# Optimization experiments

Measured on AMD Instinct MI355X. Metric: run time of the kernel, lower is better.

Reference implementation:

```python
import jax, jax.numpy as jnp
import numpy as np

HID = 768
HEADS = 12
HEAD_LEN = HID // HEADS
SCALE_INV = 1.0 / np.sqrt(HEAD_LEN).astype(np.float32)


def setup_inputs() -> dict:
    key = jax.random.key(0)
    ks = jax.random.split(key, 5)
    std = 1.0 / np.sqrt(HID)
    return {
        "x": jax.random.normal(ks[0], (1, 4096, HID), dtype=jnp.float32),
        "w_q": jax.random.normal(ks[1], (HID, HID), dtype=jnp.float32) * std,
        "w_k": jax.random.normal(ks[2], (HID, HID), dtype=jnp.float32) * std,
        "w_v": jax.random.normal(ks[3], (HID, HID), dtype=jnp.float32) * std,
        "w_fc": jax.random.normal(ks[4], (HID, HID), dtype=jnp.float32) * std,
    }


def reference(x, w_q, w_k, w_v, w_fc):
    B, S, D = x.shape
    # torch Linear weight layout [out, in]: y = x @ W.T
    def proj_heads(w):
        y = jnp.einsum("bsd,ed->bse", x, w)
        return y.reshape(B, S, HEADS, HEAD_LEN).transpose(0, 2, 1, 3)  # bhsd
    q = proj_heads(w_q)
    k = proj_heads(w_k)
    v = proj_heads(w_v)
    scores = SCALE_INV * jnp.einsum("bhqd,bhkd->bhqk", q, k)
    attn = jax.nn.softmax(scores, axis=-1)
    out = jnp.einsum("bhqk,bhkd->bhqd", attn, v)
    out = out.transpose(0, 2, 1, 3).reshape(B, S, D)
    return jnp.einsum("bsd,ed->bse", out, w_fc)
```

## Files before the change

### kernel.cpp

```cpp
#include <hip/hip_runtime.h>
#include <hip/hip_bf16.h>

#define S_LEN 4096
#define HID 768
#define NHEAD 12
#define HL 64
#define PSS 72

typedef __attribute__((ext_vector_type(8))) short short8;
typedef __attribute__((ext_vector_type(4))) float f32x4;
using bf16 = __hip_bfloat16;

__device__ __forceinline__ void gl2lds16(const void* g, void* l) {
  __builtin_amdgcn_global_load_lds((__attribute__((address_space(1))) void*)(g),
                                   (__attribute__((address_space(3))) void*)(l),
                                   16, 0, 0);
}

__device__ __forceinline__ f32x4 mfma_bf16(short8 a, short8 b, f32x4 c) {
  return __builtin_amdgcn_mfma_f32_16x16x32_bf16(a, b, c, 0, 0, 0);
}

__device__ __forceinline__ void storeC(float* C, long idx, float v) { C[idx] = v; }
__device__ __forceinline__ void storeC(bf16* C, long idx, float v) { C[idx] = __float2bfloat16(v); }

#define BAR() asm volatile("s_waitcnt lgkmcnt(0)\n\ts_barrier" ::: "memory")

__global__ __launch_bounds__(256) void cvt_all(
    const float* __restrict__ x, const float* __restrict__ wq,
    const float* __restrict__ wk, const float* __restrict__ wv,
    const float* __restrict__ wfc, bf16* __restrict__ xb, bf16* __restrict__ wqb,
    bf16* __restrict__ wkb, bf16* __restrict__ wvb, bf16* __restrict__ wfcb) {
  const long NX = (long)S_LEN * HID;
  const long NW = (long)HID * HID;
  long i = ((long)blockIdx.x * 256 + threadIdx.x) * 4;
  const float* src;
  bf16* dst;
  long off;
  if (i < NX) {
    src = x; dst = xb; off = i;
  } else {
    long j = i - NX;
    int wsel = (int)(j / NW);
    off = j - (long)wsel * NW;
    src = wsel == 0 ? wq : wsel == 1 ? wk : wsel == 2 ? wv : wfc;
    dst = wsel == 0 ? wqb : wsel == 1 ? wkb : wsel == 2 ? wvb : wfcb;
  }
  float4 v = *(const float4*)(src + off);
  bf16 h0 = __float2bfloat16(v.x), h1 = __float2bfloat16(v.y);
  bf16 h2 = __float2bfloat16(v.z), h3 = __float2bfloat16(v.w);
  ushort4 o;
  o.x = *(unsigned short*)&h0; o.y = *(unsigned short*)&h1;
  o.z = *(unsigned short*)&h2; o.w = *(unsigned short*)&h3;
  *(ushort4*)(dst + off) = o;
}

template <typename OT>
__global__ __launch_bounds__(256) void gemm_bt(
    const bf16* __restrict__ A, const bf16* __restrict__ B0,
    const bf16* __restrict__ B1, const bf16* __restrict__ B2,
    OT* __restrict__ C0, OT* __restrict__ C1, OT* __restrict__ C2, float qscale) {
  constexpr int K = HID;
  __shared__ __align__(16) bf16 As[128 * 32];
  __shared__ __align__(16) bf16 Bs[128 * 32];
  const int z = blockIdx.z;
  const bf16* B = (z == 0) ? B0 : (z == 1) ? B1 : B2;
  OT* C = (z == 0) ? C0 : (z == 1) ? C1 : C2;
  const float sc = (z == 0) ? qscale : 1.0f;
  const int bm = blockIdx.y, bn = blockIdx.x;
  const int t = threadIdx.x, lane = t & 63, w = t >> 6;
  const int wm = w >> 1, wn = w & 1;
  const int q4 = lane >> 4, c16 = lane & 15;
  const int srow = lane >> 2, scol = (lane & 3) * 8;
  const bf16* Ab = A + (long)bm * 128 * K;
  const bf16* Bb = B + (long)bn * 128 * K;
  f32x4 acc[4][4] = {};
  for (int k0 = 0; k0 < K; k0 += 32) {
#pragma unroll
    for (int r = 0; r < 2; ++r) {
      int rowb = r * 64 + w * 16;
      gl2lds16(Ab + (long)(rowb + srow) * K + k0 + scol, &As[rowb * 32]);
      gl2lds16(Bb + (long)(rowb + srow) * K + k0 + scol, &Bs[rowb * 32]);
    }
    __syncthreads();
    short8 af[4], bfv[4];
#pragma unroll
    for (int i = 0; i < 4; ++i)
      af[i] = *(const short8*)&As[(wm * 64 + i * 16 + c16) * 32 + q4 * 8];
#pragma unroll
    for (int j = 0; j < 4; ++j)
      bfv[j] = *(const short8*)&Bs[(wn * 64 + j * 16 + c16) * 32 + q4 * 8];
#pragma unroll
    for (int i = 0; i < 4; ++i)
#pragma unroll
      for (int j = 0; j < 4; ++j)
        acc[i][j] = mfma_bf16(af[i], bfv[j], acc[i][j]);
    __syncthreads();
  }
  const long crow0 = (long)bm * 128 + wm * 64;
  const int ccol0 = bn * 128 + wn * 64;
#pragma unroll
  for (int i = 0; i < 4; ++i)
#pragma unroll
    for (int j = 0; j < 4; ++j)
#pragma unroll
      for (int r = 0; r < 4; ++r) {
        long row = crow0 + i * 16 + q4 * 4 + r;
        int col = ccol0 + j * 16 + c16;
        storeC(C, row * HID + col, sc * acc[i][j][r]);
      }
}

__global__ __launch_bounds__(256) void gemm_fc(const bf16* __restrict__ A,
                                               const bf16* __restrict__ B,
                                               float* __restrict__ C) {
  __shared__ __align__(16) bf16 As[128 * 32];
  __shared__ __align__(16) bf16 Bs[64 * 32];
  const int bm = blockIdx.y, bn = blockIdx.x;
  const int t = threadIdx.x, lane = t & 63, w = t >> 6;
  const int q4 = lane >> 4, c16 = lane & 15;
  const int srow = lane >> 2, scol = (lane & 3) * 8;
  const bf16* Ab = A + (long)bm * 128 * HID;
  const bf16* Bb = B + (long)bn * 64 * HID;
  f32x4 acc[2][4] = {};
  for (int k0 = 0; k0 < HID; k0 += 32) {
#pragma unroll
    for (int r = 0; r < 2; ++r) {
      int rowb = w * 32 + r * 16;
      gl2lds16(Ab + (long)(rowb + srow) * HID + k0 + scol, &As[rowb * 32]);
    }
    gl2lds16(Bb + (long)(w * 16 + srow) * HID + k0 + scol, &Bs[w * 16 * 32]);
    __syncthreads();
    short8 af[2], bfv[4];
#pragma unroll
    for (int i = 0; i < 2; ++i)
      af[i] = *(const short8*)&As[(w * 32 + i * 16 + c16) * 32 + q4 * 8];
#pragma unroll
    for (int j = 0; j < 4; ++j)
      bfv[j] = *(const short8*)&Bs[(j * 16 + c16) * 32 + q4 * 8];
#pragma unroll
    for (int i = 0; i < 2; ++i)
#pragma unroll
      for (int j = 0; j < 4; ++j)
        acc[i][j] = mfma_bf16(af[i], bfv[j], acc[i][j]);
    __syncthreads();
  }
#pragma unroll
  for (int i = 0; i < 2; ++i)
#pragma unroll
    for (int j = 0; j < 4; ++j)
#pragma unroll
      for (int r = 0; r < 4; ++r) {
        long row = (long)bm * 128 + w * 32 + i * 16 + q4 * 4 + r;
        int col = bn * 64 + j * 16 + c16;
        C[row * HID + col] = acc[i][j][r];
      }
}

__global__ __launch_bounds__(256) void transpose_v(const bf16* __restrict__ V,
                                                   bf16* __restrict__ Vt) {
  __shared__ unsigned short tile[64][65];
  const int bs = blockIdx.x * 64;
  const int be = blockIdx.y * 64;
  const int t = threadIdx.x;
#pragma unroll
  for (int p = 0; p < 4; ++p) {
    int i = p * 256 + t;
    int r = i >> 4;
    int c = (i & 15) * 4;
    ushort4 v = *(const ushort4*)((const unsigned short*)V + (long)(bs + r) * HID + be + c);
    tile[r][c] = v.x; tile[r][c + 1] = v.y; tile[r][c + 2] = v.z; tile[r][c + 3] = v.w;
  }
  __syncthreads();
#pragma unroll
  for (int p = 0; p < 4; ++p) {
    int i = p * 256 + t;
    int r = i >> 4;
    int c = (i & 15) * 4;
    ushort4 v;
    v.x = tile[c][r]; v.y = tile[c + 1][r]; v.z = tile[c + 2][r]; v.w = tile[c + 3][r];
    *(ushort4*)((unsigned short*)Vt + (long)(be + r) * S_LEN + bs + c) = v;
  }
}

__global__ __launch_bounds__(256, 3) void flash_attn(const bf16* __restrict__ Q,
                                                     const bf16* __restrict__ Kg,
                                                     const bf16* __restrict__ Vt,
                                                     bf16* __restrict__ O) {
  __shared__ __align__(16) bf16 Ps[64 * PSS];
  __shared__ float Lred[4][64];
  const int qt = blockIdx.x, h = blockIdx.y;
  const int t = threadIdx.x, lane = t & 63, w = t >> 6;
  const int q4 = lane >> 4, c16 = lane & 15;
  const int s0 = qt * 64;

  short8 qf[2][4];
  {
    const bf16* Qb = Q + (long)(s0 + c16) * HID + h * HL + q4 * 8;
#pragma unroll
    for (int j = 0; j < 4; ++j)
#pragma unroll
      for (int ks = 0; ks < 2; ++ks)
        qf[ks][j] = *(const short8*)(Qb + (long)j * 16 * HID + ks * 32);
  }
  const bf16* kp = Kg + (long)(w * 16 + c16) * HID + h * HL + q4 * 8;
  const bf16* vp = Vt + (long)(h * HL + w * 16 + c16) * S_LEN + q4 * 8;

  float l_part[4] = {0.f, 0.f, 0.f, 0.f};
  f32x4 o_acc[4] = {};
  short8 kf0 = *(const short8*)(kp), kf1 = *(const short8*)(kp + 32);
  short8 vf0 = *(const short8*)(vp), vf1 = *(const short8*)(vp + 32);

  for (int kt = 0; kt < S_LEN / 64; ++kt) {
    f32x4 sacc[4] = {};
#pragma unroll
    for (int j = 0; j < 4; ++j) sacc[j] = mfma_bf16(kf0, qf[0][j], sacc[j]);
#pragma unroll
    for (int j = 0; j < 4; ++j) sacc[j] = mfma_bf16(kf1, qf[1][j], sacc[j]);

    const bf16* kpn = kp + 64 * HID;
    const bf16* vpn = vp + 64;
    if (kt == S_LEN / 64 - 1) { kpn = kp; vpn = vp; }
    short8 nk0 = *(const short8*)(kpn), nk1 = *(const short8*)(kpn + 32);
    short8 nv0 = *(const short8*)(vpn), nv1 = *(const short8*)(vpn + 32);

#pragma unroll
    for (int j = 0; j < 4; ++j) {
      float p0 = __builtin_amdgcn_exp2f(sacc[j][0]);
      float p1 = __builtin_amdgcn_exp2f(sacc[j][1]);
      float p2 = __builtin_amdgcn_exp2f(sacc[j][2]);
      float p3 = __builtin_amdgcn_exp2f(sacc[j][3]);
      l_part[j] += (p0 + p1) + (p2 + p3);
      bf16 b0 = __float2bfloat16(p0), b1 = __float2bfloat16(p1);
      bf16 b2 = __float2bfloat16(p2), b3 = __float2bfloat16(p3);
      short4 pk;
      pk.x = *(short*)&b0; pk.y = *(short*)&b1; pk.z = *(short*)&b2; pk.w = *(short*)&b3;
      *(short4*)&Ps[(j * 16 + c16) * PSS + w * 16 + q4 * 4] = pk;
    }
    BAR();

#pragma unroll
    for (int ks = 0; ks < 2; ++ks) {
      short8 vfk = ks ? vf1 : vf0;
#pragma unroll
      for (int j = 0; j < 4; ++j) {
        short8 pf = *(const short8*)&Ps[(j * 16 + c16) * PSS + ks * 32 + q4 * 8];
        o_acc[j] = mfma_bf16(vfk, pf, o_acc[j]);
      }
    }
    BAR();

    kf0 = nk0; kf1 = nk1; vf0 = nv0; vf1 = nv1;
    kp = kpn; vp = vpn;
  }

#pragma unroll
  for (int j = 0; j < 4; ++j) {
    float s = l_part[j];
    s += __shfl_xor(s, 16, 64);
    s += __shfl_xor(s, 32, 64);
    Lred[w][j * 16 + c16] = s;
  }
  BAR();
#pragma unroll
  for (int j = 0; j < 4; ++j) {
    int q = j * 16 + c16;
    float lt = Lred[0][q] + Lred[1][q] + Lred[2][q] + Lred[3][q];
    float rl = 1.0f / lt;
    float v0 = o_acc[j][0] * rl, v1 = o_acc[j][1] * rl;
    float v2 = o_acc[j][2] * rl, v3 = o_acc[j][3] * rl;
    bf16 b0 = __float2bfloat16(v0), b1 = __float2bfloat16(v1);
    bf16 b2 = __float2bfloat16(v2), b3 = __float2bfloat16(v3);
    short4 pk;
    pk.x = *(short*)&b0; pk.y = *(short*)&b1; pk.z = *(short*)&b2; pk.w = *(short*)&b3;
    *(short4*)&O[(long)(s0 + q) * HID + h * HL + w * 16 + q4 * 4] = pk;
  }
}

extern "C" void kernel_launch(void* const* d_in, const int* in_sizes, int n_in,
                              void* d_out, int out_size, void* d_ws, size_t ws_size,
                              hipStream_t stream) {
  const float* x = (const float*)d_in[0];
  const float* wq = (const float*)d_in[1];
  const float* wk = (const float*)d_in[2];
  const float* wv = (const float*)d_in[3];
  const float* wfc = (const float*)d_in[4];
  float* out = (float*)d_out;

  const long NBIG = (long)S_LEN * HID * sizeof(bf16);
  const long NWB = (long)HID * HID * sizeof(bf16);
  char* p = (char*)d_ws;
  bf16* xb = (bf16*)p;   p += NBIG;
  bf16* wqb = (bf16*)p;  p += NWB;
  bf16* wkb = (bf16*)p;  p += NWB;
  bf16* wvb = (bf16*)p;  p += NWB;
  bf16* wfcb = (bf16*)p; p += NWB;
  bf16* Qb = (bf16*)p;   p += NBIG;
  bf16* Kb = (bf16*)p;   p += NBIG;
  bf16* Vb = (bf16*)p;   p += NBIG;
  bf16* Vtb = (bf16*)p;  p += NBIG;
  bf16* Ob = (bf16*)p;   p += NBIG;

  const float c1 = 0.125f * 1.44269504088896340736f;

  const long total4 = ((long)S_LEN * HID + 4L * HID * HID) / 4;
  cvt_all<<<(int)(total4 / 256), 256, 0, stream>>>(x, wq, wk, wv, wfc, xb, wqb, wkb,
                                                   wvb, wfcb);
  gemm_bt<bf16><<<dim3(HID / 128, S_LEN / 128, 3), 256, 0, stream>>>(
      xb, wqb, wkb, wvb, Qb, Kb, Vb, c1);
  transpose_v<<<dim3(S_LEN / 64, HID / 64), 256, 0, stream>>>(Vb, Vtb);
  flash_attn<<<dim3(S_LEN / 64, NHEAD), 256, 0, stream>>>(Qb, Kb, Vtb, Ob);
  gemm_fc<<<dim3(HID / 64, S_LEN / 128), 256, 0, stream>>>(Ob, wfcb, out);
}
```

Measured before the change: 211.3 us.

## Keep P in registers for PV MFMA and remap blocks by XCD

New measurement: 277.3 us. 31.2% more time.

```diff
diff --git a/kernel.cpp b/kernel.cpp
--- a/kernel.cpp
+++ b/kernel.cpp
@@ -5,9 +5,11 @@
 #define HID 768
 #define NHEAD 12
 #define HL 64
-#define PSS 72
+#define QB 64
+#define ORST 68
 
 typedef __attribute__((ext_vector_type(8))) short short8;
+typedef __attribute__((ext_vector_type(4))) short s16x4;
 typedef __attribute__((ext_vector_type(4))) float f32x4;
 using bf16 = __hip_bfloat16;
 
@@ -21,10 +23,26 @@
   return __builtin_amdgcn_mfma_f32_16x16x32_bf16(a, b, c, 0, 0, 0);
 }
 
+__device__ __forceinline__ f32x4 mfma16_bf16(s16x4 a, s16x4 b, f32x4 c) {
+#if __has_builtin(__builtin_amdgcn_mfma_f32_16x16x16bf16_1k)
+  return __builtin_amdgcn_mfma_f32_16x16x16bf16_1k(a, b, c, 0, 0, 0);
+#elif __has_builtin(__builtin_amdgcn_mfma_f32_16x16x16_bf16)
+  return __builtin_amdgcn_mfma_f32_16x16x16_bf16(a, b, c, 0, 0, 0);
+#else
+  f32x4 d;
+  asm volatile(
+      "s_nop 1\n\t"
+      "v_mfma_f32_16x16x16_bf16 %0, %1, %2, %3\n\t"
+      "s_nop 7\n\t"
+      "s_nop 2"
+      : "=&v"(d)
+      : "v"(a), "v"(b), "v"(c));
+  return d;
+#endif
+}
+
 __device__ __forceinline__ void storeC(float* C, long idx, float v) { C[idx] = v; }
 __device__ __forceinline__ void storeC(bf16* C, long idx, float v) { C[idx] = __float2bfloat16(v); }
-
-#define BAR() asm volatile("s_waitcnt lgkmcnt(0)\n\ts_barrier" ::: "memory")
 
 __global__ __launch_bounds__(256) void cvt_all(
     const float* __restrict__ x, const float* __restrict__ wq,
@@ -187,12 +205,17 @@
                                                      const bf16* __restrict__ Kg,
                                                      const bf16* __restrict__ Vt,
                                                      bf16* __restrict__ O) {
-  __shared__ __align__(16) bf16 Ps[64 * PSS];
-  __shared__ float Lred[4][64];
-  const int qt = blockIdx.x, h = blockIdx.y;
+  __shared__ float Ored[64 * ORST];
+  __shared__ float Lred[4][QB];
+  const int i0 = blockIdx.x;
+  const int xcd = i0 & 7, sb = i0 >> 3;
+  const int pair = xcd >> 1;
+  const int r2 = sb * 2 + (xcd & 1);
+  const int h = pair * 3 + (r2 >> 6);
+  const int qt = r2 & 63;
   const int t = threadIdx.x, lane = t & 63, w = t >> 6;
   const int q4 = lane >> 4, c16 = lane & 15;
-  const int s0 = qt * 64;
+  const int s0 = qt * QB;
 
   short8 qf[2][4];
   {
@@ -204,25 +227,27 @@
         qf[ks][j] = *(const short8*)(Qb + (long)j * 16 * HID + ks * 32);
   }
   const bf16* kp = Kg + (long)(w * 16 + c16) * HID + h * HL + q4 * 8;
-  const bf16* vp = Vt + (long)(h * HL + w * 16 + c16) * S_LEN + q4 * 8;
+  const bf16* vbase = Vt + (long)(h * HL + c16) * S_LEN + w * 16 + q4 * 4;
 
   float l_part[4] = {0.f, 0.f, 0.f, 0.f};
-  f32x4 o_acc[4] = {};
+  f32x4 o_acc[4][4] = {};
+
   short8 kf0 = *(const short8*)(kp), kf1 = *(const short8*)(kp + 32);
-  short8 vf0 = *(const short8*)(vp), vf1 = *(const short8*)(vp + 32);
-
-  for (int kt = 0; kt < S_LEN / 64; ++kt) {
+
+  constexpr int NT = S_LEN / 64;
+  for (int kt = 0; kt < NT; ++kt) {
+    const bf16* kpn = (kt + 1 < NT) ? kp + 64 * HID : kp;
+    short8 nk0 = *(const short8*)(kpn), nk1 = *(const short8*)(kpn + 32);
+    s16x4 vf[4];
+#pragma unroll
+    for (int i = 0; i < 4; ++i)
+      vf[i] = *(const s16x4*)(vbase + (long)i * 16 * S_LEN + kt * 64);
+
     f32x4 sacc[4] = {};
 #pragma unroll
     for (int j = 0; j < 4; ++j) sacc[j] = mfma_bf16(kf0, qf[0][j], sacc[j]);
 #pragma unroll
     for (int j = 0; j < 4; ++j) sacc[j] = mfma_bf16(kf1, qf[1][j], sacc[j]);
-
-    const bf16* kpn = kp + 64 * HID;
-    const bf16* vpn = vp + 64;
-    if (kt == S_LEN / 64 - 1) { kpn = kp; vpn = vp; }
-    short8 nk0 = *(const short8*)(kpn), nk1 = *(const short8*)(kpn + 32);
-    short8 nv0 = *(const short8*)(vpn), nv1 = *(const short8*)(vpn + 32);
 
 #pragma unroll
     for (int j = 0; j < 4; ++j) {
@@ -233,25 +258,15 @@
       l_part[j] += (p0 + p1) + (p2 + p3);
       bf16 b0 = __float2bfloat16(p0), b1 = __float2bfloat16(p1);
       bf16 b2 = __float2bfloat16(p2), b3 = __float2bfloat16(p3);
-      short4 pk;
-      pk.x = *(short*)&b0; pk.y = *(short*)&b1; pk.z = *(short*)&b2; pk.w = *(short*)&b3;
-      *(short4*)&Ps[(j * 16 + c16) * PSS + w * 16 + q4 * 4] = pk;
+      s16x4 pf;
+      pf[0] = *(short*)&b0; pf[1] = *(short*)&b1;
+      pf[2] = *(short*)&b2; pf[3] = *(short*)&b3;
+#pragma unroll
+      for (int i = 0; i < 4; ++i)
+        o_acc[i][j] = mfma16_bf16(vf[i], pf, o_acc[i][j]);
     }
-    BAR();
-
-#pragma unroll
-    for (int ks = 0; ks < 2; ++ks) {
-      short8 vfk = ks ? vf1 : vf0;
-#pragma unroll
-      for (int j = 0; j < 4; ++j) {
-        short8 pf = *(const short8*)&Ps[(j * 16 + c16) * PSS + ks * 32 + q4 * 8];
-        o_acc[j] = mfma_bf16(vfk, pf, o_acc[j]);
-      }
-    }
-    BAR();
-
-    kf0 = nk0; kf1 = nk1; vf0 = nv0; vf1 = nv1;
-    kp = kpn; vp = vpn;
+
+    kf0 = nk0; kf1 = nk1; kp = kpn;
   }
 
 #pragma unroll
@@ -261,19 +276,42 @@
     s += __shfl_xor(s, 32, 64);
     Lred[w][j * 16 + c16] = s;
   }
-  BAR();
+  __syncthreads();
+  float rl[4];
 #pragma unroll
   for (int j = 0; j < 4; ++j) {
     int q = j * 16 + c16;
-    float lt = Lred[0][q] + Lred[1][q] + Lred[2][q] + Lred[3][q];
-    float rl = 1.0f / lt;
-    float v0 = o_acc[j][0] * rl, v1 = o_acc[j][1] * rl;
-    float v2 = o_acc[j][2] * rl, v3 = o_acc[j][3] * rl;
-    bf16 b0 = __float2bfloat16(v0), b1 = __float2bfloat16(v1);
-    bf16 b2 = __float2bfloat16(v2), b3 = __float2bfloat16(v3);
-    short4 pk;
-    pk.x = *(short*)&b0; pk.y = *(short*)&b1; pk.z = *(short*)&b2; pk.w = *(short*)&b3;
-    *(short4*)&O[(long)(s0 + q) * HID + h * HL + w * 16 + q4 * 4] = pk;
+    rl[j] = 1.0f / (Lred[0][q] + Lred[1][q] + Lred[2][q] + Lred[3][q]);
+  }
+
+#pragma unroll 1
+  for (int rd = 0; rd < 4; ++rd) {
+#pragma unroll
+    for (int j = 0; j < 4; ++j)
+#pragma unroll
+      for (int r = 0; r < 4; ++r)
+        Ored[(w * 16 + q4 * 4 + r) * ORST + j * 16 + c16] = o_acc[rd][j][r];
+    __syncthreads();
+    if (w == rd) {
+#pragma unroll
+      for (int j = 0; j < 4; ++j) {
+        float v[4];
+#pragma unroll
+        for (int r = 0; r < 4; ++r) {
+          int off = (q4 * 4 + r) * ORST + j * 16 + c16;
+          v[r] = (Ored[off] + Ored[16 * ORST + off]) +
+                 (Ored[32 * ORST + off] + Ored[48 * ORST + off]);
+          v[r] *= rl[j];
+        }
+        bf16 b0 = __float2bfloat16(v[0]), b1 = __float2bfloat16(v[1]);
+        bf16 b2 = __float2bfloat16(v[2]), b3 = __float2bfloat16(v[3]);
+        short4 pk;
+        pk.x = *(short*)&b0; pk.y = *(short*)&b1;
+        pk.z = *(short*)&b2; pk.w = *(short*)&b3;
+        *(short4*)&O[(long)(s0 + j * 16 + c16) * HID + h * HL + rd * 16 + q4 * 4] = pk;
+      }
+    }
+    __syncthreads();
   }
 }
 
@@ -309,6 +347,6 @@
   gemm_bt<bf16><<<dim3(HID / 128, S_LEN / 128, 3), 256, 0, stream>>>(
       xb, wqb, wkb, wvb, Qb, Kb, Vb, c1);
   transpose_v<<<dim3(S_LEN / 64, HID / 64), 256, 0, stream>>>(Vb, Vtb);
-  flash_attn<<<dim3(S_LEN / 64, NHEAD), 256, 0, stream>>>(Qb, Kb, Vtb, Ob);
+  flash_attn<<<dim3(S_LEN / QB * NHEAD), 256, 0, stream>>>(Qb, Kb, Vtb, Ob);
   gemm_fc<<<dim3(HID / 64, S_LEN / 128), 256, 0, stream>>>(Ob, wfcb, out);
 }
```
